# Kernel tuning notes

Measured on AMD Instinct MI355X. Metric: run time of the kernel, lower is better.

The kernel has to match this reference:

```python
import jax, jax.numpy as jnp
from jax import lax
import numpy as np

SHAPE = (64, 64, 64)  # spatial grid (D, H, W)
N_PTS = 100000        # active voxels
KPAD = (1, 2, 2)      # 'same' padding for (3,5,5) kernel


def _conv(x, w, pad):
    # x: [B,D,H,W,C], w: [kd,kh,kw,Cin,Cout]
    return lax.conv_general_dilated(
        x, w, window_strides=(1, 1, 1),
        padding=[(p, p) for p in pad],
        dimension_numbers=('NDHWC', 'DHWIO', 'NDHWC'))


def _sparse_maxpool2(x, mask):
    # spconv SparseMaxPool3d(2,2): output active where any input in 2x2x2
    # window is active; value = max over active inputs only.
    neg = jnp.float32(-1e30)
    xm = jnp.where(mask > 0, x, neg)
    win = (1, 2, 2, 2, 1)
    y = lax.reduce_window(xm, neg, lax.max, win, win, 'VALID')
    m2 = lax.reduce_window(mask, jnp.float32(0), lax.max, win, win, 'VALID')
    return jnp.where(m2 > 0, y, 0.0), m2


def setup_inputs() -> dict:
    rng = np.random.default_rng(0)
    D, H, W = SHAPE
    lin = rng.choice(D * H * W, size=N_PTS, replace=False)  # unique voxels
    z = lin // (H * W)
    y = (lin // W) % H
    x = lin % W
    coors = np.stack([np.zeros(N_PTS, np.int32), z, y, x], 1).astype(np.int32)

    key = jax.random.key(0)
    ks = jax.random.split(key, 16)
    feats = jax.random.normal(ks[0], (N_PTS, 3), jnp.float32)

    dims = [(3, 64), (64, 64), (64, 96), (96, 96), (96, 128), (128, 128),
            (128, 160), (160, 160), (160, 192), (192, 192), (192, 224),
            (224, 224), (224, 256), (256, 256)]
    inp = {'features': feats, 'coors': jnp.asarray(coors), 'batch_size': 1}
    for i, (ci, co) in enumerate(dims):
        scale = 1.0 / np.sqrt(ci * 75.0)  # 75 = 3*5*5 kernel taps
        inp[f'w{i}'] = jax.random.normal(ks[i + 1], (3, 5, 5, ci, co),
                                         jnp.float32) * scale
    return inp


def reference(features, coors, batch_size,
              w0, w1, w2, w3, w4, w5, w6, w7, w8, w9, w10, w11, w12, w13):
    # Densify the sparse tensor: inactive voxels are exactly zero, so a dense
    # conv followed by masking to the active set reproduces submanifold conv.
    b, z, y, x = coors[:, 0], coors[:, 1], coors[:, 2], coors[:, 3]
    dense = jnp.zeros((1,) + SHAPE + (3,), jnp.float32).at[b, z, y, x].set(features)
    mask = jnp.zeros((1,) + SHAPE + (1,), jnp.float32).at[b, z, y, x].set(1.0)

    ws = [w0, w1, w2, w3, w4, w5, w6, w7, w8, w9, w10, w11]
    h = dense
    wi = 0
    for _lvl in range(6):  # 6 (subm, subm, pool2) stages
        h = _conv(h, ws[wi], KPAD) * mask; wi += 1
        h = _conv(h, ws[wi], KPAD) * mask; wi += 1
        h, mask = _sparse_maxpool2(h, mask)

    # SparseConv3d(224,256,(3,5,5),padding=(1,2,2)): output active set is the
    # dilation of the input active set by the kernel footprint.
    m2 = lax.reduce_window(mask, jnp.float32(0), lax.max,
                           (1, 3, 5, 5, 1), (1, 1, 1, 1, 1),
                           [(0, 0), (1, 1), (2, 2), (2, 2), (0, 0)])
    h = _conv(h, w12, KPAD) * m2
    mask = m2
    # final SubMConv3d(256,256)
    h = _conv(h, w13, KPAD) * mask
    return h  # [1,1,1,1,256]
```

## Files before the change

### kernel.cpp

```cpp
#include <hip/hip_runtime.h>
#include <hip/hip_bf16.h>
#include <cstdint>

typedef __attribute__((ext_vector_type(8))) short bf16x8;
typedef __attribute__((ext_vector_type(4))) float f32x4;

__device__ __forceinline__ unsigned short f2bf_hi(float v) {
    unsigned u = __float_as_uint(v);
    u = u + 0x7fffu + ((u >> 16) & 1u);
    return (unsigned short)(u >> 16);
}
__device__ __forceinline__ float bf2f(unsigned short h) {
    return __uint_as_float(((unsigned)h) << 16);
}

__global__ void scatter_kernel(const float* __restrict__ feats,
                               const int* __restrict__ coors,
                               float* __restrict__ dense,
                               float* __restrict__ mask, int n)
{
    int i = blockIdx.x * blockDim.x + threadIdx.x;
    if (i >= n) return;
    const int z = coors[i * 4 + 1];
    const int y = coors[i * 4 + 2];
    const int x = coors[i * 4 + 3];
    const size_t s = (size_t)((z * 64 + y) * 64 + x);
    dense[s * 3 + 0] = feats[i * 3 + 0];
    dense[s * 3 + 1] = feats[i * 3 + 1];
    dense[s * 3 + 2] = feats[i * 3 + 2];
    mask[s] = 1.f;
}

__global__ void wprep_kernel(const float* __restrict__ w,
                             unsigned short* __restrict__ wv, int CI, int CO)
{
    const int total = 75 * CI * CO;
    const int stride = gridDim.x * blockDim.x;
    for (int i = blockIdx.x * blockDim.x + threadIdx.x; i < total; i += stride) {
        const int tap = i / (CI * CO);
        const int r = i - tap * CI * CO;
        const int ci = r / CO;
        const int co = r - ci * CO;
        const size_t o = ((size_t)(tap * (CI / 8) + (ci >> 3)) * CO + co) * 8 + (ci & 7);
        wv[o] = f2bf_hi(w[i]);
    }
}

__global__ void wprep2_kernel(const float* __restrict__ w,
                              unsigned short* __restrict__ wv, int CI, int CO)
{
    const int total = 75 * CI * CO;
    const int stride = gridDim.x * blockDim.x;
    for (int i = blockIdx.x * blockDim.x + threadIdx.x; i < total; i += stride) {
        const int tap = i / (CI * CO);
        const int r = i - tap * CI * CO;
        const int ci = r / CO;
        const int co = r - ci * CO;
        const float v = w[i];
        const unsigned short h = f2bf_hi(v);
        const unsigned short l = f2bf_hi(v - bf2f(h));
        const size_t o = ((size_t)(tap * (CI / 8) + (ci >> 3)) * CO + co) * 16 + (ci & 7);
        wv[o] = h; wv[o + 8] = l;
    }
}

__global__ __launch_bounds__(256)
void conv1_kernel(const float* __restrict__ in, const float* __restrict__ w,
                  const float* __restrict__ mask, unsigned short* __restrict__ ob)
{
    constexpr int S = 64, SP = 68;
    __shared__ float lds[15][3][SP];

    const int bid = blockIdx.y * S + blockIdx.x;
    const int wg = (bid & 7) * (S * S / 8) + (bid >> 3);
    const int y = wg & 63, z = wg >> 6;
    const int t = threadIdx.x;

    for (int idx = t; idx < 15 * 3 * SP; idx += 256) {
        const int r = idx / (3 * SP);
        const int rem = idx - r * 3 * SP;
        const int ci = rem / SP;
        const int x = rem - ci * SP;
        const int kz = r / 5, ky = r - kz * 5;
        const int zz = z + kz - 1, yy = y + ky - 2, xi = x - 2;
        float v = 0.f;
        if ((unsigned)zz < (unsigned)S && (unsigned)yy < (unsigned)S && (unsigned)xi < (unsigned)S)
            v = in[(size_t)((zz * S + yy) * S + xi) * 3 + ci];
        lds[r][ci][x] = v;
    }
    __syncthreads();

    const int co = t & 63, xs = t >> 6;
    float acc[16];
#pragma unroll
    for (int i = 0; i < 16; ++i) acc[i] = 0.f;

#pragma unroll 1
    for (int r = 0; r < 15; ++r) {
#pragma unroll
        for (int ci = 0; ci < 3; ++ci) {
            float inv[20];
#pragma unroll
            for (int j = 0; j < 5; ++j)
                *(float4*)&inv[j * 4] = *(const float4*)&lds[r][ci][xs * 16 + j * 4];
            const float* wp = w + (size_t)(r * 15 + ci) * 64 + co;
#pragma unroll
            for (int kx = 0; kx < 5; ++kx) {
                const float wv = wp[kx * 192];
#pragma unroll
                for (int i = 0; i < 16; ++i) acc[i] += inv[i + kx] * wv;
            }
        }
    }

    const size_t vb = (size_t)(z * S + y) * S;
#pragma unroll
    for (int i = 0; i < 16; ++i) {
        const int x = xs * 16 + i;
        const float keep = (mask[vb + x] > 0.f) ? 1.f : 0.f;
        ob[(vb + x) * 64 + co] = f2bf_hi(acc[i] * keep);
    }
}

template<int CIN, int COUT, int S, int YB, int YG, int WN, int NG, int OMODE>
__global__ __launch_bounds__(YG * NG * 64)
void mfma_conv6(const unsigned short* __restrict__ ab,
                const unsigned short* __restrict__ wv,
                const float* __restrict__ mask, float* __restrict__ outf,
                unsigned short* __restrict__ outb)
{
    constexpr int SP = S + 4;
    constexpr int MX = S / 16;
    constexpr int KC = CIN / 32;
    constexpr int KC4 = CIN / 8;
    constexpr int RS = (KC4 <= 8) ? 8 : 16;
    constexpr int PLANE = SP * RS;
    constexpr int NL = SP * KC4;
    constexpr int NW = YG * NG;
    constexpr int NT = NW * 64;
    constexpr int SREG = (NL + NT - 1) / NT;
    constexpr int YBW = YB / YG;
    constexpr int NYB = S / YB;
    constexpr int NP = 3 * (YB + 4);
    static_assert(COUT / 16 == WN * NG, "geometry");

    __shared__ unsigned short lds[2 * PLANE * 8];

    const int bid = blockIdx.y * NYB + blockIdx.x;
    constexpr int NWG = NYB * S;
    const int wg = (bid & 7) * (NWG / 8) + (bid >> 3);
    const int yb = wg % NYB, z = wg / NYB;
    const int y0 = yb * YB;

    const int t = threadIdx.x;
    const int lane = t & 63;
    const int wave = t >> 6;
    const int waveN = wave % NG;
    const int waveY = wave / NG;
    const int col = lane & 15;
    const int ci8 = lane >> 4;

    f32x4 acc[YBW][MX][WN];
    const f32x4 vzero = {0.f, 0.f, 0.f, 0.f};
#pragma unroll
    for (int q = 0; q < YBW; ++q)
#pragma unroll
        for (int m = 0; m < MX; ++m)
#pragma unroll
            for (int n = 0; n < WN; ++n) acc[q][m][n] = vzero;

    uint4 reg[SREG];

    auto issue = [&](int ph) {
        const int kz = ph / (YB + 4), j = ph - kz * (YB + 4);
        const int zz = z + kz - 1, yy = y0 + j - 2;
        const bool rv = ((unsigned)zz < (unsigned)S) && ((unsigned)yy < (unsigned)S);
        const size_t rowbase = rv ? (size_t)((zz * S + yy) * S) * CIN : 0;
#pragma unroll
        for (int i = 0; i < SREG; ++i) {
            const int L = i * NT + t;
            uint4 v = {0u, 0u, 0u, 0u};
            if (L < NL) {
                const int x = L / KC4;
                const int c3 = L - x * KC4;
                const int xi = x - 2;
                if (rv && (unsigned)xi < (unsigned)S)
                    v = *(const uint4*)(ab + rowbase + (size_t)xi * CIN + c3 * 8);
            }
            reg[i] = v;
        }
    };
    auto store = [&](int pl) {
#pragma unroll
        for (int i = 0; i < SREG; ++i) {
            const int L = i * NT + t;
            if (L < NL) {
                const int x = L / KC4;
                const int c3 = L - x * KC4;
                const int p = x * RS + (c3 ^ (x & 7));
                *(uint4*)&lds[(pl * PLANE + p) * 8] = reg[i];
            }
        }
    };

    issue(0);
    store(0);
    if (NP > 1) issue(1);
    __syncthreads();

    int cur = 0;
#pragma unroll 1
    for (int ph = 0; ph < NP; ++ph) {
        const int kz = ph / (YB + 4), j = ph - kz * (YB + 4);
        const int zz = z + kz - 1, yy = y0 + j - 2;
        if (((unsigned)zz < (unsigned)S) && ((unsigned)yy < (unsigned)S)) {
            const unsigned short* plane = lds + cur * PLANE * 8;

            bool vq[YBW];
            int tapb[YBW];
#pragma unroll
            for (int ql = 0; ql < YBW; ++ql) {
                const int q = waveY * YBW + ql;
                const int ky = j - q;
                vq[ql] = (ky >= 0 && ky <= 4);
                tapb[ql] = (kz * 5 + (vq[ql] ? ky : 0)) * 5;
            }

            bf16x8 wA[YBW][KC][WN], wB[YBW][KC][WN];
            auto wload = [&](bf16x8 (&wb)[YBW][KC][WN], int kx) {
#pragma unroll
                for (int ql = 0; ql < YBW; ++ql) if (vq[ql]) {
                    const int tap = tapb[ql] + kx;
#pragma unroll
                    for (int kc = 0; kc < KC; ++kc) {
                        const int c3 = kc * 4 + ci8;
#pragma unroll
                        for (int n = 0; n < WN; ++n) {
                            const int co = (waveN * WN + n) * 16 + col;
                            wb[ql][kc][n] = *(const bf16x8*)(wv + ((size_t)(tap * KC4 + c3) * COUT + co) * 8);
                        }
                    }
                }
            };
            auto wmfma = [&](bf16x8 (&wb)[YBW][KC][WN], bf16x8 (&a)[KC][MX]) {
#pragma unroll
                for (int ql = 0; ql < YBW; ++ql) if (vq[ql])
#pragma unroll
                    for (int kc = 0; kc < KC; ++kc)
#pragma unroll
                        for (int m = 0; m < MX; ++m)
#pragma unroll
                            for (int n = 0; n < WN; ++n)
                                acc[ql][m][n] = __builtin_amdgcn_mfma_f32_16x16x32_bf16(a[kc][m], wb[ql][kc][n], acc[ql][m][n], 0, 0, 0);
            };

            wload(wA, 0);
            __builtin_amdgcn_s_setprio(1);
#pragma unroll
            for (int kx = 0; kx < 5; ++kx) {
                bf16x8 a[KC][MX];
#pragma unroll
                for (int kc = 0; kc < KC; ++kc) {
                    const int c3 = kc * 4 + ci8;
#pragma unroll
                    for (int m = 0; m < MX; ++m) {
                        const int x = m * 16 + col + kx;
                        const int p = x * RS + (c3 ^ (x & 7));
                        a[kc][m] = *(const bf16x8*)&plane[p * 8];
                    }
                }
                if ((kx & 1) == 0) {
                    if (kx + 1 < 5) wload(wB, kx + 1);
                    wmfma(wA, a);
                } else {
                    if (kx + 1 < 5) wload(wA, kx + 1);
                    wmfma(wB, a);
                }
            }
            __builtin_amdgcn_s_setprio(0);
        }
        if (ph + 1 < NP) store(cur ^ 1);
        if (ph + 2 < NP) issue(ph + 2);
        __syncthreads();
        cur ^= 1;
    }

    const int rq = lane >> 4;
#pragma unroll
    for (int ql = 0; ql < YBW; ++ql) {
        const int y = y0 + waveY * YBW + ql;
        const size_t vb = (size_t)(z * S + y) * S;
#pragma unroll
        for (int m = 0; m < MX; ++m) {
            const int xb = m * 16 + rq * 4;
#pragma unroll
            for (int r = 0; r < 4; ++r) {
                const int x = xb + r;
                const float keep = (mask[vb + x] > 0.f) ? 1.f : 0.f;
#pragma unroll
                for (int n = 0; n < WN; ++n) {
                    const int co = (waveN * WN + n) * 16 + col;
                    const float v = acc[ql][m][n][r] * keep;
                    if (OMODE == 0) outf[(vb + x) * COUT + co] = v;
                    else            outb[(vb + x) * COUT + co] = f2bf_hi(v);
                }
            }
        }
    }
}

template<int CIN, int COUT, int S, int WM, int WN, int MG, int NG, int OMODE>
__global__ __launch_bounds__(MG * NG * 64)
void mfma_conv3c(const unsigned short* __restrict__ ab,
                 const unsigned short* __restrict__ wv,
                 const float* __restrict__ mask, float* __restrict__ outf,
                 unsigned short* __restrict__ outb)
{
    constexpr int SP = S + 4;
    constexpr int KC = CIN / 32;
    constexpr int KC4 = CIN / 8;
    constexpr int RS = (KC4 <= 8) ? 8 : 16;
    constexpr int PLANE = SP * RS;
    constexpr int NL = SP * KC4;
    constexpr int NT = MG * NG * 64;
    constexpr int SREG = (NL + NT - 1) / NT;
    static_assert(S / 16 == WM * MG && COUT / 16 == WN * NG, "geometry");

    __shared__ unsigned short lds[2 * PLANE * 8];

    const int bid = blockIdx.y * S + blockIdx.x;
    const int wg = (bid & 7) * (S * S / 8) + (bid >> 3);
    const int y = wg % S, z = wg / S;

    const int t = threadIdx.x;
    const int lane = t & 63;
    const int wave = t >> 6;
    const int waveM = wave % MG;
    const int waveN = wave / MG;
    const int col = lane & 15;
    const int ci8 = lane >> 4;

    f32x4 acc[WM][WN];
    const f32x4 vzero = {0.f, 0.f, 0.f, 0.f};
#pragma unroll
    for (int m = 0; m < WM; ++m)
#pragma unroll
        for (int n = 0; n < WN; ++n) acc[m][n] = vzero;

    uint4 reg[SREG];

    auto issue = [&](int kzy) {
        const int kz = kzy / 5, ky = kzy - kz * 5;
        const int zz = z + kz - 1, yy = y + ky - 2;
        const bool rv = ((unsigned)zz < (unsigned)S) && ((unsigned)yy < (unsigned)S);
        const size_t rowbase = rv ? (size_t)((zz * S + yy) * S) * CIN : 0;
#pragma unroll
        for (int i = 0; i < SREG; ++i) {
            const int L = i * NT + t;
            uint4 v = {0u, 0u, 0u, 0u};
            if (L < NL) {
                const int x = L / KC4;
                const int c3 = L - x * KC4;
                const int xi = x - 2;
                if (rv && (unsigned)xi < (unsigned)S)
                    v = *(const uint4*)(ab + rowbase + (size_t)xi * CIN + c3 * 8);
            }
            reg[i] = v;
        }
    };
    auto store = [&](int pl) {
#pragma unroll
        for (int i = 0; i < SREG; ++i) {
            const int L = i * NT + t;
            if (L < NL) {
                const int x = L / KC4;
                const int c3 = L - x * KC4;
                const int p = x * RS + (c3 ^ (x & 7));
                *(uint4*)&lds[(pl * PLANE + p) * 8] = reg[i];
            }
        }
    };

    issue(0);
    store(0);
    issue(1);
    __syncthreads();

    int cur = 0;
#pragma unroll 1
    for (int kzy = 0; kzy < 15; ++kzy) {
        const int kz = kzy / 5, ky = kzy - kz * 5;
        const int zz = z + kz - 1, yy = y + ky - 2;
        if (((unsigned)zz < (unsigned)S) && ((unsigned)yy < (unsigned)S)) {
            const unsigned short* plane = lds + cur * PLANE * 8;

            bf16x8 wA[KC][WN], wB[KC][WN];
            auto wload = [&](bf16x8 (&wb)[KC][WN], int kx) {
                const int tap = kzy * 5 + kx;
#pragma unroll
                for (int kc = 0; kc < KC; ++kc) {
                    const int c3 = kc * 4 + ci8;
#pragma unroll
                    for (int n = 0; n < WN; ++n) {
                        const int co = (waveN * WN + n) * 16 + col;
                        wb[kc][n] = *(const bf16x8*)(wv + ((size_t)(tap * KC4 + c3) * COUT + co) * 8);
                    }
                }
            };
            auto wmfma = [&](bf16x8 (&wb)[KC][WN], bf16x8 (&a)[KC][WM]) {
#pragma unroll
                for (int kc = 0; kc < KC; ++kc)
#pragma unroll
                    for (int m = 0; m < WM; ++m)
#pragma unroll
                        for (int n = 0; n < WN; ++n)
                            acc[m][n] = __builtin_amdgcn_mfma_f32_16x16x32_bf16(a[kc][m], wb[kc][n], acc[m][n], 0, 0, 0);
            };

            wload(wA, 0);
            __builtin_amdgcn_s_setprio(1);
#pragma unroll
            for (int kx = 0; kx < 5; ++kx) {
                bf16x8 a[KC][WM];
#pragma unroll
                for (int kc = 0; kc < KC; ++kc) {
                    const int c3 = kc * 4 + ci8;
#pragma unroll
                    for (int m = 0; m < WM; ++m) {
                        const int x = (waveM * WM + m) * 16 + col + kx;
                        const int p = x * RS + (c3 ^ (x & 7));
                        a[kc][m] = *(const bf16x8*)&plane[p * 8];
                    }
                }
                if ((kx & 1) == 0) {
                    if (kx + 1 < 5) wload(wB, kx + 1);
                    wmfma(wA, a);
                } else {
                    if (kx + 1 < 5) wload(wA, kx + 1);
                    wmfma(wB, a);
                }
            }
            __builtin_amdgcn_s_setprio(0);
        }
        if (kzy + 1 < 15) store(cur ^ 1);
        if (kzy + 2 < 15) issue(kzy + 2);
        __syncthreads();
        cur ^= 1;
    }

    const int rq = lane >> 4;
    const size_t vb = (size_t)(z * S + y) * S;
#pragma unroll
    for (int m = 0; m < WM; ++m) {
        const int xb = (waveM * WM + m) * 16 + rq * 4;
#pragma unroll
        for (int r = 0; r < 4; ++r) {
            const int x = xb + r;
            const float keep = (mask[vb + x] > 0.f) ? 1.f : 0.f;
#pragma unroll
            for (int n = 0; n < WN; ++n) {
                const int co = (waveN * WN + n) * 16 + col;
                const float v = acc[m][n][r] * keep;
                if (OMODE == 0) outf[(vb + x) * COUT + co] = v;
                else            outb[(vb + x) * COUT + co] = f2bf_hi(v);
            }
        }
    }
}

template<int CIN, int COUT, int S, int NW>
__global__ __launch_bounds__(NW * 64)
void dgemm2_kernel(const unsigned short* __restrict__ inb,
                   const unsigned short* __restrict__ wv,
                   const float* __restrict__ mask,
                   unsigned short* __restrict__ outb)
{
    constexpr int M = S * S * S;
    constexpr int KC = CIN / 32;
    constexpr int KC4 = CIN / 8;
    __shared__ f32x4 part[NW][64];

    const int t = threadIdx.x;
    const int lane = t & 63;
    const int w = t >> 6;
    const int col = lane & 15;
    const int g = lane >> 4;

    const int va = blockIdx.x * 16 + col;
    const bool av = (va < M);
    const int az = (va / (S * S)) % S;
    const int ay = (va / S) % S;
    const int ax = va % S;
    const int co = blockIdx.y * 16 + col;

    f32x4 acc0 = {0.f, 0.f, 0.f, 0.f};
    f32x4 acc1 = {0.f, 0.f, 0.f, 0.f};

#pragma unroll 2
    for (int tap = w; tap < 75; tap += NW) {
        const int dz = tap / 25 - 1;
        const int dy = (tap / 5) % 5 - 2;
        const int dx = tap % 5 - 2;
        const int zz = az + dz, yy = ay + dy, xx = ax + dx;
        const bool valid = av && ((unsigned)zz < (unsigned)S) &&
                           ((unsigned)yy < (unsigned)S) && ((unsigned)xx < (unsigned)S);
        const size_t abase = valid ? (size_t)((zz * S + yy) * S + xx) * CIN : 0;
#pragma unroll
        for (int kc = 0; kc < KC; ++kc) {
            const int c3 = kc * 4 + g;
            bf16x8 a = {0, 0, 0, 0, 0, 0, 0, 0};
            if (valid) a = *(const bf16x8*)(inb + abase + c3 * 8);
            const unsigned short* wp = wv + ((size_t)(tap * KC4 + c3) * COUT + co) * 16;
            bf16x8 wh = *(const bf16x8*)wp;
            bf16x8 wl = *(const bf16x8*)(wp + 8);
            acc0 = __builtin_amdgcn_mfma_f32_16x16x32_bf16(a, wh, acc0, 0, 0, 0);
            acc1 = __builtin_amdgcn_mfma_f32_16x16x32_bf16(a, wl, acc1, 0, 0, 0);
        }
    }

    part[w][lane] = acc0 + acc1;
    __syncthreads();

    if (w == 0) {
        f32x4 s = part[0][lane];
#pragma unroll
        for (int i = 1; i < NW; ++i) s += part[i][lane];
#pragma unroll
        for (int r = 0; r < 4; ++r) {
            const int v = blockIdx.x * 16 + g * 4 + r;
            if (v < M) {
                const float keep = (mask[v] > 0.f) ? 1.f : 0.f;
                outb[(size_t)v * COUT + co] = f2bf_hi(s[r] * keep);
            }
        }
    }
}

__global__ void pool_bf8_kernel(const unsigned short* __restrict__ inb,
                                const float* __restrict__ mi,
                                unsigned short* __restrict__ outb,
                                float* __restrict__ mo, int S, int C)
{
    const int So = S >> 1;
    const int C8 = C >> 3;
    const long long total = (long long)So * So * So * C8;
    for (long long i = blockIdx.x * (long long)blockDim.x + threadIdx.x; i < total;
         i += (long long)gridDim.x * blockDim.x) {
        const int c8 = (int)(i % C8);
        const long long s = i / C8;
        const int xo = (int)(s % So);
        const int yo = (int)((s / So) % So);
        const int zo = (int)(s / ((long long)So * So));
        float best[8];
#pragma unroll
        for (int k = 0; k < 8; ++k) best[k] = -1e30f;
        float m2 = 0.f;
        for (int dz = 0; dz < 2; ++dz)
            for (int dy = 0; dy < 2; ++dy)
                for (int dx = 0; dx < 2; ++dx) {
                    const int zi = zo * 2 + dz, yi = yo * 2 + dy, xi = xo * 2 + dx;
                    const float m = mi[(zi * S + yi) * S + xi];
                    if (m > 0.f) {
                        m2 = 1.f;
                        const unsigned short* p =
                            inb + ((size_t)((zi * S + yi) * S + xi) * C8 + c8) * 8;
                        uint4 v = *(const uint4*)p;
                        const unsigned short* vs = (const unsigned short*)&v;
#pragma unroll
                        for (int k = 0; k < 8; ++k) best[k] = fmaxf(best[k], bf2f(vs[k]));
                    }
                }
        uint4 o;
        unsigned short* os = (unsigned short*)&o;
#pragma unroll
        for (int k = 0; k < 8; ++k) os[k] = f2bf_hi((m2 > 0.f) ? best[k] : 0.f);
        *(uint4*)(outb + i * 8) = o;
        if (c8 == 0) mo[s] = m2;
    }
}

__global__ __launch_bounds__(256)
void final_kernel(const unsigned short* __restrict__ h, const float* __restrict__ mask,
                  const float* __restrict__ w12, const float* __restrict__ w13,
                  float* __restrict__ out)
{
    __shared__ float o1[256];
    const int co = threadIdx.x;
    const float m = (mask[0] > 0.f) ? 1.f : 0.f;
    float a = 0.f;
    for (int ci = 0; ci < 224; ++ci)
        a += bf2f(h[ci]) * w12[(size_t)(37 * 224 + ci) * 256 + co];
    o1[co] = a * m;
    __syncthreads();
    float b = 0.f;
    for (int ci = 0; ci < 256; ++ci)
        b += o1[ci] * w13[(size_t)(37 * 256 + ci) * 256 + co];
    out[co] = b * m;
}

static void pool_bf8(const unsigned short* inb, const float* mi,
                     unsigned short* outb, float* mo, int S, int C, hipStream_t stream)
{
    const long long total = (long long)(S / 2) * (S / 2) * (S / 2) * (C / 8);
    long long grid = (total + 255) / 256;
    if (grid > 4096) grid = 4096;
    if (grid < 1) grid = 1;
    pool_bf8_kernel<<<(int)grid, 256, 0, stream>>>(inb, mi, outb, mo, S, C);
}

#define WOFF0 0
#define WOFF1 307200
#define WOFF2 768000
#define WOFF3 1459200
#define WOFF4 2380800
#define DOFF6 0
#define DOFF7 3072000
#define DOFF8 6912000
#define DOFF9 11520000
#define DOFF10 17049600
#define DOFF11 23500800

extern "C" void kernel_launch(void* const* d_in, const int* in_sizes, int n_in,
                              void* d_out, int out_size, void* d_ws, size_t ws_size,
                              hipStream_t stream)
{
    const float* feats = (const float*)d_in[0];
    const int*   coors = (const int*)d_in[1];
    const float* w[14];
    for (int i = 0; i < 14; ++i) w[i] = (const float*)d_in[3 + i];
    float* outp = (float*)d_out;

    float* dense0 = (float*)d_ws;
    float* mA = dense0 + 786432;
    float* mB = mA + 262144;
    unsigned short* ab = (unsigned short*)(mB + 262144);
    unsigned short* bb = ab + 16777216;
    unsigned short* wvp = bb + 16777216;
    unsigned short* wdp = wvp + 3609600;

    const int npts = in_sizes[0] / 3;

    wprep_kernel<<<256, 256, 0, stream>>>(w[1], wvp + WOFF0, 64, 64);
    wprep_kernel<<<256, 256, 0, stream>>>(w[2], wvp + WOFF1, 64, 96);
    wprep_kernel<<<256, 256, 0, stream>>>(w[3], wvp + WOFF2, 96, 96);
    wprep_kernel<<<256, 256, 0, stream>>>(w[4], wvp + WOFF3, 96, 128);
    wprep_kernel<<<256, 256, 0, stream>>>(w[5], wvp + WOFF4, 128, 128);
    wprep2_kernel<<<256, 256, 0, stream>>>(w[6], wdp + DOFF6, 128, 160);
    wprep2_kernel<<<256, 256, 0, stream>>>(w[7], wdp + DOFF7, 160, 160);
    wprep2_kernel<<<256, 256, 0, stream>>>(w[8], wdp + DOFF8, 160, 192);
    wprep2_kernel<<<256, 256, 0, stream>>>(w[9], wdp + DOFF9, 192, 192);
    wprep2_kernel<<<256, 256, 0, stream>>>(w[10], wdp + DOFF10, 192, 224);
    wprep2_kernel<<<256, 256, 0, stream>>>(w[11], wdp + DOFF11, 224, 224);

    hipMemsetAsync(dense0, 0, (size_t)786432 * sizeof(float), stream);
    hipMemsetAsync(mA, 0, (size_t)262144 * sizeof(float), stream);
    scatter_kernel<<<(npts + 255) / 256, 256, 0, stream>>>(feats, coors, dense0, mA, npts);

    conv1_kernel<<<dim3(64, 64), 256, 0, stream>>>(dense0, w[0], mA, ab);
    mfma_conv6<64, 64, 64, 4, 2, 2, 2, 1><<<dim3(16, 64), 256, 0, stream>>>(
        ab, wvp + WOFF0, mA, nullptr, bb);
    pool_bf8(bb, mA, ab, mB, 64, 64, stream);
    mfma_conv6<64, 96, 32, 2, 1, 2, 3, 1><<<dim3(16, 32), 192, 0, stream>>>(
        ab, wvp + WOFF1, mB, nullptr, bb);
    mfma_conv6<96, 96, 32, 2, 1, 2, 3, 1><<<dim3(16, 32), 192, 0, stream>>>(
        bb, wvp + WOFF2, mB, nullptr, ab);
    pool_bf8(ab, mB, bb, mA, 32, 96, stream);
    mfma_conv3c<96, 128, 16, 1, 2, 1, 4, 1><<<dim3(16, 16), 256, 0, stream>>>(
        bb, wvp + WOFF3, mA, nullptr, ab);
    mfma_conv3c<128, 128, 16, 1, 2, 1, 4, 1><<<dim3(16, 16), 256, 0, stream>>>(
        ab, wvp + WOFF4, mA, nullptr, bb);
    pool_bf8(bb, mA, ab, mB, 16, 128, stream);
    dgemm2_kernel<128, 160, 8, 4><<<dim3(32, 10), 256, 0, stream>>>(ab, wdp + DOFF6, mB, bb);
    dgemm2_kernel<160, 160, 8, 4><<<dim3(32, 10), 256, 0, stream>>>(bb, wdp + DOFF7, mB, ab);
    pool_bf8(ab, mB, bb, mA, 8, 160, stream);
    dgemm2_kernel<160, 192, 4, 8><<<dim3(4, 12), 512, 0, stream>>>(bb, wdp + DOFF8, mA, ab);
    dgemm2_kernel<192, 192, 4, 8><<<dim3(4, 12), 512, 0, stream>>>(ab, wdp + DOFF9, mA, bb);
    pool_bf8(bb, mA, ab, mB, 4, 192, stream);
    dgemm2_kernel<192, 224, 2, 8><<<dim3(1, 14), 512, 0, stream>>>(ab, wdp + DOFF10, mB, bb);
    dgemm2_kernel<224, 224, 2, 8><<<dim3(1, 14), 512, 0, stream>>>(bb, wdp + DOFF11, mB, ab);
    pool_bf8(ab, mB, bb, mA, 2, 224, stream);
    final_kernel<<<1, 256, 0, stream>>>(bb, mA, w[12], w[13], outp);
}
```

Baseline: 849.4 us.

## Stage two y-rows per pipeline phase in MFMA conv and retile level-2 convs

The MFMA submanifold conv kernel now loads two input y-rows into shared memory per pipeline phase instead of one. This halves the number of phases and __syncthreads barriers, and each barrier interval has more MFMA work to overlap with the global loads. The level-2 convs (64->96, 96->96) are also retiled from YB=2 with 3 waves to YB=4 with 4 waves in a 2x2 layout. The cost is double the LDS footprint and more staging registers, which may reduce occupancy.

```diff
diff --git a/kernel.cpp b/kernel.cpp
--- a/kernel.cpp
+++ b/kernel.cpp
@@ -124,7 +124,7 @@
 
 template<int CIN, int COUT, int S, int YB, int YG, int WN, int NG, int OMODE>
 __global__ __launch_bounds__(YG * NG * 64)
-void mfma_conv6(const unsigned short* __restrict__ ab,
+void mfma_conv7(const unsigned short* __restrict__ ab,
                 const unsigned short* __restrict__ wv,
                 const float* __restrict__ mask, float* __restrict__ outf,
                 unsigned short* __restrict__ outb)
@@ -135,16 +135,19 @@
     constexpr int KC4 = CIN / 8;
     constexpr int RS = (KC4 <= 8) ? 8 : 16;
     constexpr int PLANE = SP * RS;
-    constexpr int NL = SP * KC4;
+    constexpr int NLR = SP * KC4;
+    constexpr int NL = 2 * NLR;
     constexpr int NW = YG * NG;
     constexpr int NT = NW * 64;
     constexpr int SREG = (NL + NT - 1) / NT;
     constexpr int YBW = YB / YG;
     constexpr int NYB = S / YB;
-    constexpr int NP = 3 * (YB + 4);
+    constexpr int JP = (YB + 4) / 2;
+    constexpr int NP = 3 * JP;
     static_assert(COUT / 16 == WN * NG, "geometry");
-
-    __shared__ unsigned short lds[2 * PLANE * 8];
+    static_assert((YB + 4) % 2 == 0, "YB even");
+
+    __shared__ unsigned short lds[2 * 2 * PLANE * 8];
 
     const int bid = blockIdx.y * NYB + blockIdx.x;
     constexpr int NWG = NYB * S;
@@ -172,20 +175,22 @@
     uint4 reg[SREG];
 
     auto issue = [&](int ph) {
-        const int kz = ph / (YB + 4), j = ph - kz * (YB + 4);
-        const int zz = z + kz - 1, yy = y0 + j - 2;
-        const bool rv = ((unsigned)zz < (unsigned)S) && ((unsigned)yy < (unsigned)S);
-        const size_t rowbase = rv ? (size_t)((zz * S + yy) * S) * CIN : 0;
+        const int kz = ph / JP, jp = ph - kz * JP;
+        const int zz = z + kz - 1;
+        const bool zv = ((unsigned)zz < (unsigned)S);
 #pragma unroll
         for (int i = 0; i < SREG; ++i) {
             const int L = i * NT + t;
             uint4 v = {0u, 0u, 0u, 0u};
             if (L < NL) {
-                const int x = L / KC4;
-                const int c3 = L - x * KC4;
+                const int jr = L / NLR;
+                const int l2 = L - jr * NLR;
+                const int x = l2 / KC4;
+                const int c3 = l2 - x * KC4;
                 const int xi = x - 2;
-                if (rv && (unsigned)xi < (unsigned)S)
-                    v = *(const uint4*)(ab + rowbase + (size_t)xi * CIN + c3 * 8);
+                const int yy = y0 + jp * 2 + jr - 2;
+                if (zv && (unsigned)yy < (unsigned)S && (unsigned)xi < (unsigned)S)
+                    v = *(const uint4*)(ab + (size_t)((zz * S + yy) * S + xi) * CIN + c3 * 8);
             }
             reg[i] = v;
         }
@@ -195,10 +200,12 @@
         for (int i = 0; i < SREG; ++i) {
             const int L = i * NT + t;
             if (L < NL) {
-                const int x = L / KC4;
-                const int c3 = L - x * KC4;
+                const int jr = L / NLR;
+                const int l2 = L - jr * NLR;
+                const int x = l2 / KC4;
+                const int c3 = l2 - x * KC4;
                 const int p = x * RS + (c3 ^ (x & 7));
-                *(uint4*)&lds[(pl * PLANE + p) * 8] = reg[i];
+                *(uint4*)&lds[((pl * 2 + jr) * PLANE + p) * 8] = reg[i];
             }
         }
     };
@@ -211,73 +218,79 @@
     int cur = 0;
 #pragma unroll 1
     for (int ph = 0; ph < NP; ++ph) {
-        const int kz = ph / (YB + 4), j = ph - kz * (YB + 4);
-        const int zz = z + kz - 1, yy = y0 + j - 2;
-        if (((unsigned)zz < (unsigned)S) && ((unsigned)yy < (unsigned)S)) {
-            const unsigned short* plane = lds + cur * PLANE * 8;
-
-            bool vq[YBW];
-            int tapb[YBW];
-#pragma unroll
-            for (int ql = 0; ql < YBW; ++ql) {
-                const int q = waveY * YBW + ql;
-                const int ky = j - q;
-                vq[ql] = (ky >= 0 && ky <= 4);
-                tapb[ql] = (kz * 5 + (vq[ql] ? ky : 0)) * 5;
-            }
-
-            bf16x8 wA[YBW][KC][WN], wB[YBW][KC][WN];
-            auto wload = [&](bf16x8 (&wb)[YBW][KC][WN], int kx) {
-#pragma unroll
-                for (int ql = 0; ql < YBW; ++ql) if (vq[ql]) {
-                    const int tap = tapb[ql] + kx;
+        const int kz = ph / JP, jp = ph - kz * JP;
+        const int zz = z + kz - 1;
+        if ((unsigned)zz < (unsigned)S) {
+#pragma unroll
+            for (int jr = 0; jr < 2; ++jr) {
+                const int j = jp * 2 + jr;
+                const int yy = y0 + j - 2;
+                if ((unsigned)yy >= (unsigned)S) continue;
+                const unsigned short* plane = lds + (cur * 2 + jr) * PLANE * 8;
+
+                bool vq[YBW];
+                int tapb[YBW];
+#pragma unroll
+                for (int ql = 0; ql < YBW; ++ql) {
+                    const int q = waveY * YBW + ql;
+                    const int ky = j - q;
+                    vq[ql] = (ky >= 0 && ky <= 4);
+                    tapb[ql] = (kz * 5 + (vq[ql] ? ky : 0)) * 5;
+                }
+
+                bf16x8 wA[YBW][KC][WN], wB[YBW][KC][WN];
+                auto wload = [&](bf16x8 (&wb)[YBW][KC][WN], int kx) {
+#pragma unroll
+                    for (int ql = 0; ql < YBW; ++ql) if (vq[ql]) {
+                        const int tap = tapb[ql] + kx;
+#pragma unroll
+                        for (int kc = 0; kc < KC; ++kc) {
+                            const int c3 = kc * 4 + ci8;
+#pragma unroll
+                            for (int n = 0; n < WN; ++n) {
+                                const int co = (waveN * WN + n) * 16 + col;
+                                wb[ql][kc][n] = *(const bf16x8*)(wv + ((size_t)(tap * KC4 + c3) * COUT + co) * 8);
+                            }
+                        }
+                    }
+                };
+                auto wmfma = [&](bf16x8 (&wb)[YBW][KC][WN], bf16x8 (&a)[KC][MX]) {
+#pragma unroll
+                    for (int ql = 0; ql < YBW; ++ql) if (vq[ql])
+#pragma unroll
+                        for (int kc = 0; kc < KC; ++kc)
+#pragma unroll
+                            for (int m = 0; m < MX; ++m)
+#pragma unroll
+                                for (int n = 0; n < WN; ++n)
+                                    acc[ql][m][n] = __builtin_amdgcn_mfma_f32_16x16x32_bf16(a[kc][m], wb[ql][kc][n], acc[ql][m][n], 0, 0, 0);
+                };
+
+                wload(wA, 0);
+                __builtin_amdgcn_s_setprio(1);
+#pragma unroll
+                for (int kx = 0; kx < 5; ++kx) {
+                    bf16x8 a[KC][MX];
 #pragma unroll
                     for (int kc = 0; kc < KC; ++kc) {
                         const int c3 = kc * 4 + ci8;
 #pragma unroll
-                        for (int n = 0; n < WN; ++n) {
-                            const int co = (waveN * WN + n) * 16 + col;
-                            wb[ql][kc][n] = *(const bf16x8*)(wv + ((size_t)(tap * KC4 + c3) * COUT + co) * 8);
+                        for (int m = 0; m < MX; ++m) {
+                            const int x = m * 16 + col + kx;
+                            const int p = x * RS + (c3 ^ (x & 7));
+                            a[kc][m] = *(const bf16x8*)&plane[p * 8];
                         }
                     }
-                }
-            };
-            auto wmfma = [&](bf16x8 (&wb)[YBW][KC][WN], bf16x8 (&a)[KC][MX]) {
-#pragma unroll
-                for (int ql = 0; ql < YBW; ++ql) if (vq[ql])
-#pragma unroll
-                    for (int kc = 0; kc < KC; ++kc)
-#pragma unroll
-                        for (int m = 0; m < MX; ++m)
-#pragma unroll
-                            for (int n = 0; n < WN; ++n)
-                                acc[ql][m][n] = __builtin_amdgcn_mfma_f32_16x16x32_bf16(a[kc][m], wb[ql][kc][n], acc[ql][m][n], 0, 0, 0);
-            };
-
-            wload(wA, 0);
-            __builtin_amdgcn_s_setprio(1);
-#pragma unroll
-            for (int kx = 0; kx < 5; ++kx) {
-                bf16x8 a[KC][MX];
-#pragma unroll
-                for (int kc = 0; kc < KC; ++kc) {
-                    const int c3 = kc * 4 + ci8;
-#pragma unroll
-                    for (int m = 0; m < MX; ++m) {
-                        const int x = m * 16 + col + kx;
-                        const int p = x * RS + (c3 ^ (x & 7));
-                        a[kc][m] = *(const bf16x8*)&plane[p * 8];
+                    if ((kx & 1) == 0) {
+                        if (kx + 1 < 5) wload(wB, kx + 1);
+                        wmfma(wA, a);
+                    } else {
+                        if (kx + 1 < 5) wload(wA, kx + 1);
+                        wmfma(wB, a);
                     }
                 }
-                if ((kx & 1) == 0) {
-                    if (kx + 1 < 5) wload(wB, kx + 1);
-                    wmfma(wA, a);
-                } else {
-                    if (kx + 1 < 5) wload(wA, kx + 1);
-                    wmfma(wB, a);
-                }
-            }
-            __builtin_amdgcn_s_setprio(0);
+                __builtin_amdgcn_s_setprio(0);
+            }
         }
         if (ph + 1 < NP) store(cur ^ 1);
         if (ph + 2 < NP) issue(ph + 2);
@@ -657,12 +670,12 @@
     scatter_kernel<<<(npts + 255) / 256, 256, 0, stream>>>(feats, coors, dense0, mA, npts);
 
     conv1_kernel<<<dim3(64, 64), 256, 0, stream>>>(dense0, w[0], mA, ab);
-    mfma_conv6<64, 64, 64, 4, 2, 2, 2, 1><<<dim3(16, 64), 256, 0, stream>>>(
+    mfma_conv7<64, 64, 64, 4, 2, 2, 2, 1><<<dim3(16, 64), 256, 0, stream>>>(
         ab, wvp + WOFF0, mA, nullptr, bb);
     pool_bf8(bb, mA, ab, mB, 64, 64, stream);
-    mfma_conv6<64, 96, 32, 2, 1, 2, 3, 1><<<dim3(16, 32), 192, 0, stream>>>(
+    mfma_conv7<64, 96, 32, 4, 2, 3, 2, 1><<<dim3(8, 32), 256, 0, stream>>>(
         ab, wvp + WOFF1, mB, nullptr, bb);
-    mfma_conv6<96, 96, 32, 2, 1, 2, 3, 1><<<dim3(16, 32), 192, 0, stream>>>(
+    mfma_conv7<96, 96, 32, 4, 2, 3, 2, 1><<<dim3(8, 32), 256, 0, stream>>>(
         bb, wvp + WOFF2, mB, nullptr, ab);
     pool_bf8(ab, mB, bb, mA, 32, 96, stream);
     mfma_conv3c<96, 128, 16, 1, 2, 1, 4, 1><<<dim3(16, 16), 256, 0, stream>>>(
```

Result: no change. 865.0 us (+1.8%).
